# Optimization experiments

Measured on AMD Instinct MI355X. Metric: run time of the kernel, lower is better.

Reference implementation:

```python
import jax, jax.numpy as jnp
import numpy as np

N_QUBITS = 7
N_LAYERS = 2
HILBERT = 2 ** N_QUBITS


def _rx(t):
    c = jnp.cos(t / 2).astype(jnp.complex64)
    s = (-1j * jnp.sin(t / 2)).astype(jnp.complex64)
    return jnp.stack([jnp.stack([c, s]), jnp.stack([s, c])])


def _ry(t):
    c = jnp.cos(t / 2).astype(jnp.complex64)
    s = jnp.sin(t / 2).astype(jnp.complex64)
    return jnp.stack([jnp.stack([c, -s]), jnp.stack([s, c])])


def _rz(t):
    z0 = jnp.exp(-0.5j * t).astype(jnp.complex64)
    z1 = jnp.exp(0.5j * t).astype(jnp.complex64)
    zero = jnp.zeros_like(z0)
    return jnp.stack([jnp.stack([z0, zero]), jnp.stack([zero, z1])])


def _apply_1q(state, U, q):
    # state: [B, 2, 2, ..., 2]; wire q lives on axis q+1 (wire 0 = MSB, PennyLane convention)
    ax = q + 1
    out = jnp.tensordot(U, state, axes=[[1], [ax]])  # new gate axis at 0
    return jnp.moveaxis(out, 0, ax)


def _apply_cnot(state, c, t):
    c_ax, t_ax = c + 1, t + 1
    s0 = jax.lax.index_in_dim(state, 0, c_ax, keepdims=False)
    s1 = jax.lax.index_in_dim(state, 1, c_ax, keepdims=False)
    t2 = t_ax - 1 if t_ax > c_ax else t_ax  # target axis after control axis removed
    s1 = jnp.flip(s1, axis=t2)  # X on target within control=1 block
    return jnp.stack([s0, s1], axis=c_ax)


def setup_inputs() -> dict:
    key = jax.random.key(0)
    k1, k2 = jax.random.split(key)
    x = jax.random.normal(k1, (131072, HILBERT), dtype=jnp.float32)
    weights = jax.random.uniform(k2, (N_LAYERS, N_QUBITS, 3), dtype=jnp.float32) * (2 * np.pi)
    return {"x": x, "weights": weights}


def reference(x, weights):
    B = x.shape[0]
    norms = jnp.maximum(jnp.linalg.norm(x, axis=-1, keepdims=True), 1e-8)
    psi = (x / norms).astype(jnp.complex64)
    state = psi.reshape((B,) + (2,) * N_QUBITS)
    for layer in range(N_LAYERS):
        for q in range(N_QUBITS):
            state = _apply_1q(state, _rx(weights[layer, q, 0]), q)
            state = _apply_1q(state, _ry(weights[layer, q, 1]), q)
            state = _apply_1q(state, _rz(weights[layer, q, 2]), q)
        for q in range(N_QUBITS):
            state = _apply_cnot(state, q, (q + 1) % N_QUBITS)
    probs = jnp.abs(state) ** 2  # real [B, 2,...,2]
    zs = []
    for q in range(N_QUBITS):
        other = tuple(a for a in range(1, N_QUBITS + 1) if a != q + 1)
        p = probs.sum(axis=other)  # [B, 2] marginal of wire q
        zs.append(p[:, 0] - p[:, 1])
    return jnp.stack(zs, axis=-1)  # [B, N_QUBITS]
```

## Files before the change

kernel.cpp:

```cpp
#include <hip/hip_runtime.h>
#include <hip/hip_bf16.h>


typedef __attribute__((ext_vector_type(8)))  short short8;
typedef __attribute__((ext_vector_type(16))) float f32x16;

static __device__ __forceinline__ short f2bf(float f) {
  __bf16 h = (__bf16)f;
  return __builtin_bit_cast(short, h);
}

static __device__ __forceinline__ int widx(int P, int s, int k) {
  return ((((P << 2) + (s >> 5)) * 8 + (k >> 4)) * 64 +
          ((s & 31) + ((k >> 3) & 1) * 32)) * 8 + (k & 7);
}

__global__ void qnn_build_w(const float* __restrict__ wts,
                            short* __restrict__ W) {
  const int k = blockIdx.x;
  const int l = threadIdx.x;

  float c0r = (2 * l     == k) ? 1.f : 0.f, c0i = 0.f;
  float c1r = (2 * l + 1 == k) ? 1.f : 0.f, c1i = 0.f;

  for (int layer = 0; layer < 2; ++layer) {
    for (int q = 0; q < 7; ++q) {
      const float t0 = 0.5f * wts[(layer * 7 + q) * 3 + 0];
      const float t1 = 0.5f * wts[(layer * 7 + q) * 3 + 1];
      const float t2 = 0.5f * wts[(layer * 7 + q) * 3 + 2];
      const float cx = __cosf(t0), sx = __sinf(t0);
      const float cy = __cosf(t1), sy = __sinf(t1);
      const float cz = __cosf(t2), sz = __sinf(t2);
      const float m00r =  cy * cx, m00i =  sy * sx;
      const float m01r = -sy * cx, m01i = -cy * sx;
      const float m10r =  sy * cx, m10i = -cy * sx;
      const float m11r =  cy * cx, m11i = -sy * sx;
      const float g00r = m00r * cz + m00i * sz, g00i = m00i * cz - m00r * sz;
      const float g01r = m01r * cz + m01i * sz, g01i = m01i * cz - m01r * sz;
      const float g10r = m10r * cz - m10i * sz, g10i = m10i * cz + m10r * sz;
      const float g11r = m11r * cz - m11i * sz, g11i = m11i * cz + m11r * sz;

      const int b = 6 - q;
      if (b == 0) {
        const float n0r = g00r*c0r - g00i*c0i + g01r*c1r - g01i*c1i;
        const float n0i = g00r*c0i + g00i*c0r + g01r*c1i + g01i*c1r;
        const float n1r = g10r*c0r - g10i*c0i + g11r*c1r - g11i*c1i;
        const float n1i = g10r*c0i + g10i*c0r + g11r*c1i + g11i*c1r;
        c0r = n0r; c0i = n0i; c1r = n1r; c1i = n1i;
      } else {
        const int xm  = 1 << (b - 1);
        const int myb = (l >> (b - 1)) & 1;
        const float p0r = __shfl_xor(c0r, xm), p0i = __shfl_xor(c0i, xm);
        const float p1r = __shfl_xor(c1r, xm), p1i = __shfl_xor(c1i, xm);
        const float gar = myb ? g11r : g00r, gai = myb ? g11i : g00i;
        const float gbr = myb ? g10r : g01r, gbi = myb ? g10i : g01i;
        const float n0r = gar*c0r - gai*c0i + gbr*p0r - gbi*p0i;
        const float n0i = gar*c0i + gai*c0r + gbr*p0i + gbi*p0r;
        const float n1r = gar*c1r - gai*c1i + gbr*p1r - gbi*p1i;
        const float n1i = gar*c1i + gai*c1r + gbr*p1i + gbi*p1r;
        c0r = n0r; c0i = n0i; c1r = n1r; c1i = n1i;
      }
    }
    #pragma unroll
    for (int q = 0; q < 7; ++q) {
      const int bc = 6 - q;
      const int bt = 6 - ((q + 1) % 7);
      if (bt == 0) {
        if (l & 1) { float tr=c0r, ti=c0i; c0r=c1r; c0i=c1i; c1r=tr; c1i=ti; }
      } else if (bc == 0) {
        c1r = __shfl_xor(c1r, 32);
        c1i = __shfl_xor(c1i, 32);
      } else {
        const int xm = 1 << (bt - 1);
        const float p0r = __shfl_xor(c0r, xm), p0i = __shfl_xor(c0i, xm);
        const float p1r = __shfl_xor(c1r, xm), p1i = __shfl_xor(c1i, xm);
        if ((l >> (bc - 1)) & 1) { c0r=p0r; c0i=p0i; c1r=p1r; c1i=p1i; }
      }
    }
  }

  W[widx(0, 2 * l,     k)] = f2bf(c0r);
  W[widx(0, 2 * l + 1, k)] = f2bf(c1r);
  W[widx(1, 2 * l,     k)] = f2bf(c0i);
  W[widx(1, 2 * l + 1, k)] = f2bf(c1i);
}

__global__ __launch_bounds__(256, 4) void qnn_main(
    const float* __restrict__ x, const short* __restrict__ W,
    float* __restrict__ out) {
  const int tid = threadIdx.x;
  const int l   = tid & 63;
  const int wv  = tid >> 6;
  const int col = l & 31;
  const int h   = l >> 5;

  __shared__ short8 xb[1024];
  __shared__ float  red[4][64][7];

  const int t0 = blockIdx.x;

  float4 fa[4], fb[4];
  #pragma unroll
  for (int i = 0; i < 4; ++i) {
    const int p = i * 256 + tid;
    const int r = p >> 4, q = p & 15;
    const float* gp = x + (size_t)(t0 * 64 + r) * 128 + q * 8;
    fa[i] = *reinterpret_cast<const float4*>(gp);
    fb[i] = *reinterpret_cast<const float4*>(gp + 4);
  }

  short8 A0[8], A1[8];
  #pragma unroll
  for (int j = 0; j < 8; ++j) {
    const int off = ((wv * 8 + j) * 64 + l) * 8;
    A0[j] = *reinterpret_cast<const short8*>(W + off);
    A1[j] = *reinterpret_cast<const short8*>(W + 16384 + off);
  }

  #pragma unroll
  for (int i = 0; i < 4; ++i) {
    const int p = i * 256 + tid;
    const int r = p >> 4, q = p & 15;
    short8 c;
    c[0]=f2bf(fa[i].x); c[1]=f2bf(fa[i].y); c[2]=f2bf(fa[i].z); c[3]=f2bf(fa[i].w);
    c[4]=f2bf(fb[i].x); c[5]=f2bf(fb[i].y); c[6]=f2bf(fb[i].z); c[7]=f2bf(fb[i].w);
    xb[r * 16 + (q ^ (r & 7))] = c;
  }
  asm volatile("s_waitcnt lgkmcnt(0)" ::: "memory");
  __builtin_amdgcn_s_barrier();
  asm volatile("" ::: "memory");

  #pragma unroll
  for (int g = 0; g < 2; ++g) {
    f32x16 acc0 = {0.f,0.f,0.f,0.f,0.f,0.f,0.f,0.f,
                   0.f,0.f,0.f,0.f,0.f,0.f,0.f,0.f};
    f32x16 acc1 = {0.f,0.f,0.f,0.f,0.f,0.f,0.f,0.f,
                   0.f,0.f,0.f,0.f,0.f,0.f,0.f,0.f};
    const int r = g * 32 + col;
    #pragma unroll
    for (int j = 0; j < 8; ++j) {
      const int q = j * 2 + h;
      const short8 bfr = xb[r * 16 + (q ^ (r & 7))];
      acc0 = __builtin_amdgcn_mfma_f32_32x32x16_bf16(A0[j], bfr, acc0, 0, 0, 0);
      acc1 = __builtin_amdgcn_mfma_f32_32x32x16_bf16(A1[j], bfr, acc1, 0, 0, 0);
    }
    float aS[8], aD[8];
    #pragma unroll
    for (int i = 0; i < 8; ++i) {
      const float pe = acc0[2*i]   * acc0[2*i]   + acc1[2*i]   * acc1[2*i];
      const float po = acc0[2*i+1] * acc0[2*i+1] + acc1[2*i+1] * acc1[2*i+1];
      aS[i] = pe + po;
      aD[i] = pe - po;
    }
    float bS[4], bD[4];
    #pragma unroll
    for (int i = 0; i < 4; ++i) {
      bS[i] = aS[2*i] + aS[2*i+1];
      bD[i] = aS[2*i] - aS[2*i+1];
    }
    float u0 = ((aD[0]+aD[1]) + (aD[2]+aD[3])) + ((aD[4]+aD[5]) + (aD[6]+aD[7]));
    float u1 = (bD[0] + bD[1]) + (bD[2] + bD[3]);
    const float cS0 = bS[0] + bS[1], cD0 = bS[0] - bS[1];
    const float cS1 = bS[2] + bS[3], cD1 = bS[2] - bS[3];
    float u3 = cD0 + cD1;
    float u4 = cS0 - cS1;
    float T  = cS0 + cS1;

    const float Tp = __shfl_xor(T, 32);
    const float u2 = h ? (Tp - T) : (T - Tp);
    T += Tp;
    u0 += __shfl_xor(u0, 32);
    u1 += __shfl_xor(u1, 32);
    u3 += __shfl_xor(u3, 32);
    u4 += __shfl_xor(u4, 32);

    if (h == 0) {
      red[wv][r][0] = T;
      red[wv][r][1] = u0;
      red[wv][r][2] = u1;
      red[wv][r][3] = u2;
      red[wv][r][4] = u3;
      red[wv][r][5] = u4;
    }
  }

  asm volatile("s_waitcnt lgkmcnt(0)" ::: "memory");
  __builtin_amdgcn_s_barrier();
  asm volatile("" ::: "memory");

  if (tid < 64) {
    const int c = tid;
    const float T0 = red[0][c][0], T1 = red[1][c][0];
    const float T2 = red[2][c][0], T3 = red[3][c][0];
    const float sT  = (T0 + T1) + (T2 + T3);
    const float inv = 1.0f / sT;
    const float z0 = (T0 + T1) - (T2 + T3);
    const float z1 = (T0 - T1) + (T2 - T3);
    float zr[5];
    #pragma unroll
    for (int i = 0; i < 5; ++i)
      zr[i] = (red[0][c][5-i] + red[1][c][5-i]) +
              (red[2][c][5-i] + red[3][c][5-i]);
    float* o = out + (size_t)(t0 * 64 + c) * 7;
    o[0] = z0 * inv; o[1] = z1 * inv; o[2] = zr[0] * inv; o[3] = zr[1] * inv;
    o[4] = zr[2] * inv; o[5] = zr[3] * inv; o[6] = zr[4] * inv;
  }
}

extern "C" void kernel_launch(void* const* d_in, const int* in_sizes, int n_in,
                              void* d_out, int out_size, void* d_ws, size_t ws_size,
                              hipStream_t stream) {
  const float* x   = (const float*)d_in[0];
  const float* wts = (const float*)d_in[1];
  float* out = (float*)d_out;
  short* W   = (short*)d_ws;

  const int B     = in_sizes[0] / 128;
  const int grid  = B / 64;

  qnn_build_w<<<128, 64, 0, stream>>>(wts, W);
  qnn_main<<<grid, 256, 0, stream>>>(x, W, out);
}
```

Baseline: 24.05 us.

## Double-buffer x tiles in LDS via async global_load_lds across a persistent loop

```diff
diff --git a/kernel.cpp b/kernel.cpp
--- a/kernel.cpp
+++ b/kernel.cpp
@@ -8,6 +8,12 @@
 static __device__ __forceinline__ short f2bf(float f) {
   __bf16 h = (__bf16)f;
   return __builtin_bit_cast(short, h);
+}
+
+static __device__ __forceinline__ void gl16(const void* g, void* l) {
+  __builtin_amdgcn_global_load_lds(
+      (const __attribute__((address_space(1))) void*)g,
+      (__attribute__((address_space(3))) void*)l, 16, 0, 0);
 }
 
 static __device__ __forceinline__ int widx(int P, int s, int k) {
@@ -87,27 +93,18 @@
 
 __global__ __launch_bounds__(256, 4) void qnn_main(
     const float* __restrict__ x, const short* __restrict__ W,
-    float* __restrict__ out) {
+    float* __restrict__ out, int ntiles) {
   const int tid = threadIdx.x;
   const int l   = tid & 63;
   const int wv  = tid >> 6;
   const int col = l & 31;
   const int h   = l >> 5;
 
-  __shared__ short8 xb[1024];
-  __shared__ float  red[4][64][7];
-
-  const int t0 = blockIdx.x;
-
-  float4 fa[4], fb[4];
-  #pragma unroll
-  for (int i = 0; i < 4; ++i) {
-    const int p = i * 256 + tid;
-    const int r = p >> 4, q = p & 15;
-    const float* gp = x + (size_t)(t0 * 64 + r) * 128 + q * 8;
-    fa[i] = *reinterpret_cast<const float4*>(gp);
-    fb[i] = *reinterpret_cast<const float4*>(gp + 4);
-  }
+  __shared__ float xb[2][4096];
+  __shared__ float red[4][32][7];
+
+  const int T0 = blockIdx.x * 4;
+  const int NT = min(4, ntiles - T0);
 
   short8 A0[8], A1[8];
   #pragma unroll
@@ -117,93 +114,119 @@
     A1[j] = *reinterpret_cast<const short8*>(W + 16384 + off);
   }
 
-  #pragma unroll
-  for (int i = 0; i < 4; ++i) {
-    const int p = i * 256 + tid;
-    const int r = p >> 4, q = p & 15;
-    short8 c;
-    c[0]=f2bf(fa[i].x); c[1]=f2bf(fa[i].y); c[2]=f2bf(fa[i].z); c[3]=f2bf(fa[i].w);
-    c[4]=f2bf(fb[i].x); c[5]=f2bf(fb[i].y); c[6]=f2bf(fb[i].z); c[7]=f2bf(fb[i].w);
-    xb[r * 16 + (q ^ (r & 7))] = c;
-  }
-  asm volatile("s_waitcnt lgkmcnt(0)" ::: "memory");
-  __builtin_amdgcn_s_barrier();
-  asm volatile("" ::: "memory");
-
-  #pragma unroll
-  for (int g = 0; g < 2; ++g) {
+  auto ISSUE = [&](int T, int b) {
+    const char* gbase = (const char*)(x + (size_t)T * 32 * 128);
+    char* lbase = (char*)&xb[b][0];
+    #pragma unroll
+    for (int i = 0; i < 4; ++i) {
+      const int d   = i * 4096 + tid * 16;
+      const int r   = d >> 9;
+      const int c16 = (d >> 4) & 31;
+      const int q32 = c16 >> 1, hf = c16 & 1;
+      const int qg  = q32 ^ (r & 7);
+      const int hg  = hf  ^ ((r >> 3) & 1);
+      gl16(gbase + r * 512 + qg * 32 + hg * 16, lbase + d);
+    }
+  };
+
+  if (NT > 0) ISSUE(T0, 0);
+  if (NT > 1) ISSUE(T0 + 1, 1);
+
+  for (int i = 0; i < NT; ++i) {
+    const int p = i & 1;
+
+    if (i + 1 < NT) { asm volatile("s_waitcnt vmcnt(4)" ::: "memory"); }
+    else            { asm volatile("s_waitcnt vmcnt(0)" ::: "memory"); }
+    __builtin_amdgcn_s_barrier();
+    asm volatile("" ::: "memory");
+
     f32x16 acc0 = {0.f,0.f,0.f,0.f,0.f,0.f,0.f,0.f,
                    0.f,0.f,0.f,0.f,0.f,0.f,0.f,0.f};
     f32x16 acc1 = {0.f,0.f,0.f,0.f,0.f,0.f,0.f,0.f,
                    0.f,0.f,0.f,0.f,0.f,0.f,0.f,0.f};
-    const int r = g * 32 + col;
-    #pragma unroll
-    for (int j = 0; j < 8; ++j) {
-      const int q = j * 2 + h;
-      const short8 bfr = xb[r * 16 + (q ^ (r & 7))];
-      acc0 = __builtin_amdgcn_mfma_f32_32x32x16_bf16(A0[j], bfr, acc0, 0, 0, 0);
-      acc1 = __builtin_amdgcn_mfma_f32_32x32x16_bf16(A1[j], bfr, acc1, 0, 0, 0);
-    }
-    float aS[8], aD[8];
-    #pragma unroll
-    for (int i = 0; i < 8; ++i) {
-      const float pe = acc0[2*i]   * acc0[2*i]   + acc1[2*i]   * acc1[2*i];
-      const float po = acc0[2*i+1] * acc0[2*i+1] + acc1[2*i+1] * acc1[2*i+1];
-      aS[i] = pe + po;
-      aD[i] = pe - po;
-    }
-    float bS[4], bD[4];
-    #pragma unroll
-    for (int i = 0; i < 4; ++i) {
-      bS[i] = aS[2*i] + aS[2*i+1];
-      bD[i] = aS[2*i] - aS[2*i+1];
-    }
-    float u0 = ((aD[0]+aD[1]) + (aD[2]+aD[3])) + ((aD[4]+aD[5]) + (aD[6]+aD[7]));
-    float u1 = (bD[0] + bD[1]) + (bD[2] + bD[3]);
-    const float cS0 = bS[0] + bS[1], cD0 = bS[0] - bS[1];
-    const float cS1 = bS[2] + bS[3], cD1 = bS[2] - bS[3];
-    float u3 = cD0 + cD1;
-    float u4 = cS0 - cS1;
-    float T  = cS0 + cS1;
-
-    const float Tp = __shfl_xor(T, 32);
-    const float u2 = h ? (Tp - T) : (T - Tp);
-    T += Tp;
-    u0 += __shfl_xor(u0, 32);
-    u1 += __shfl_xor(u1, 32);
-    u3 += __shfl_xor(u3, 32);
-    u4 += __shfl_xor(u4, 32);
-
-    if (h == 0) {
-      red[wv][r][0] = T;
-      red[wv][r][1] = u0;
-      red[wv][r][2] = u1;
-      red[wv][r][3] = u2;
-      red[wv][r][4] = u3;
-      red[wv][r][5] = u4;
-    }
-  }
-
-  asm volatile("s_waitcnt lgkmcnt(0)" ::: "memory");
-  __builtin_amdgcn_s_barrier();
-  asm volatile("" ::: "memory");
-
-  if (tid < 64) {
-    const int c = tid;
-    const float T0 = red[0][c][0], T1 = red[1][c][0];
-    const float T2 = red[2][c][0], T3 = red[3][c][0];
-    const float sT  = (T0 + T1) + (T2 + T3);
-    const float inv = 1.0f / sT;
-    const float z0 = (T0 + T1) - (T2 + T3);
-    const float z1 = (T0 - T1) + (T2 - T3);
-    float zr[5];
-    #pragma unroll
-    for (int i = 0; i < 5; ++i)
-      zr[i] = (red[0][c][5-i] + red[1][c][5-i]) +
-              (red[2][c][5-i] + red[3][c][5-i]);
-    float* o = out + (size_t)(t0 * 64 + c) * 7;
-    o[0] = z0 * inv; o[1] = z1 * inv; o[2] = zr[0] * inv; o[3] = zr[1] * inv;
-    o[4] = zr[2] * inv; o[5] = zr[3] * inv; o[6] = zr[4] * inv;
+    {
+      const int hb = (col >> 3) & 1;
+      const char* xrow = (const char*)&xb[p][0] + col * 512;
+      #pragma unroll
+      for (int j = 0; j < 8; ++j) {
+        const int qg  = j * 2 + h;
+        const int q32 = qg ^ (col & 7);
+        const float4 f0 = *reinterpret_cast<const float4*>(
+            xrow + q32 * 32 + hb * 16);
+        const float4 f1 = *reinterpret_cast<const float4*>(
+            xrow + q32 * 32 + (hb ^ 1) * 16);
+        short8 bfr;
+        bfr[0]=f2bf(f0.x); bfr[1]=f2bf(f0.y); bfr[2]=f2bf(f0.z); bfr[3]=f2bf(f0.w);
+        bfr[4]=f2bf(f1.x); bfr[5]=f2bf(f1.y); bfr[6]=f2bf(f1.z); bfr[7]=f2bf(f1.w);
+        acc0 = __builtin_amdgcn_mfma_f32_32x32x16_bf16(A0[j], bfr, acc0, 0, 0, 0);
+        acc1 = __builtin_amdgcn_mfma_f32_32x32x16_bf16(A1[j], bfr, acc1, 0, 0, 0);
+      }
+    }
+
+    {
+      float aS[8], aD[8];
+      #pragma unroll
+      for (int i2 = 0; i2 < 8; ++i2) {
+        const float pe = acc0[2*i2]   * acc0[2*i2]   + acc1[2*i2]   * acc1[2*i2];
+        const float po = acc0[2*i2+1] * acc0[2*i2+1] + acc1[2*i2+1] * acc1[2*i2+1];
+        aS[i2] = pe + po;
+        aD[i2] = pe - po;
+      }
+      float bS[4], bD[4];
+      #pragma unroll
+      for (int i2 = 0; i2 < 4; ++i2) {
+        bS[i2] = aS[2*i2] + aS[2*i2+1];
+        bD[i2] = aS[2*i2] - aS[2*i2+1];
+      }
+      float u0 = ((aD[0]+aD[1]) + (aD[2]+aD[3])) + ((aD[4]+aD[5]) + (aD[6]+aD[7]));
+      float u1 = (bD[0] + bD[1]) + (bD[2] + bD[3]);
+      const float cS0 = bS[0] + bS[1], cD0 = bS[0] - bS[1];
+      const float cS1 = bS[2] + bS[3], cD1 = bS[2] - bS[3];
+      float u3 = cD0 + cD1;
+      float u4 = cS0 - cS1;
+      float T  = cS0 + cS1;
+
+      const float Tp = __shfl_xor(T, 32);
+      const float u2 = h ? (Tp - T) : (T - Tp);
+      T += Tp;
+      u0 += __shfl_xor(u0, 32);
+      u1 += __shfl_xor(u1, 32);
+      u3 += __shfl_xor(u3, 32);
+      u4 += __shfl_xor(u4, 32);
+
+      if (h == 0) {
+        red[wv][col][0] = T;
+        red[wv][col][1] = u0;
+        red[wv][col][2] = u1;
+        red[wv][col][3] = u2;
+        red[wv][col][4] = u3;
+        red[wv][col][5] = u4;
+      }
+    }
+
+    asm volatile("s_waitcnt lgkmcnt(0)" ::: "memory");
+    __builtin_amdgcn_s_barrier();
+    asm volatile("" ::: "memory");
+
+    if (tid < 32) {
+      const int c = tid;
+      const float T0v = red[0][c][0], T1v = red[1][c][0];
+      const float T2v = red[2][c][0], T3v = red[3][c][0];
+      const float sT  = (T0v + T1v) + (T2v + T3v);
+      const float inv = 1.0f / sT;
+      const float z0 = (T0v + T1v) - (T2v + T3v);
+      const float z1 = (T0v - T1v) + (T2v - T3v);
+      float zr[5];
+      #pragma unroll
+      for (int i2 = 0; i2 < 5; ++i2)
+        zr[i2] = (red[0][c][5-i2] + red[1][c][5-i2]) +
+                 (red[2][c][5-i2] + red[3][c][5-i2]);
+      float* o = out + (size_t)((T0 + i) * 32 + c) * 7;
+      o[0] = z0 * inv; o[1] = z1 * inv; o[2] = zr[0] * inv; o[3] = zr[1] * inv;
+      o[4] = zr[2] * inv; o[5] = zr[3] * inv; o[6] = zr[4] * inv;
+    }
+
+    if (i + 2 < NT) ISSUE(T0 + i + 2, p);
   }
 }
 
@@ -215,9 +238,10 @@
   float* out = (float*)d_out;
   short* W   = (short*)d_ws;
 
-  const int B     = in_sizes[0] / 128;
-  const int grid  = B / 64;
+  const int B      = in_sizes[0] / 128;
+  const int ntiles = B / 32;
+  const int grid   = (ntiles + 3) / 4;
 
   qnn_build_w<<<128, 64, 0, stream>>>(wts, W);
-  qnn_main<<<grid, 256, 0, stream>>>(x, W, out);
-}
+  qnn_main<<<grid, 256, 0, stream>>>(x, W, out, ntiles);
+}
```

New measurement: 31.37 us. 1.3x slower.

## Stage fp32 input tile into LDS via direct global-to-LDS loads

Applied to the files above, without the earlier changes.

```diff
diff --git a/kernel.cpp b/kernel.cpp
--- a/kernel.cpp
+++ b/kernel.cpp
@@ -8,6 +8,12 @@
 static __device__ __forceinline__ short f2bf(float f) {
   __bf16 h = (__bf16)f;
   return __builtin_bit_cast(short, h);
+}
+
+static __device__ __forceinline__ void gl16(const void* g, void* l) {
+  __builtin_amdgcn_global_load_lds(
+      (const __attribute__((address_space(1))) void*)g,
+      (__attribute__((address_space(3))) void*)l, 16, 0, 0);
 }
 
 static __device__ __forceinline__ int widx(int P, int s, int k) {
@@ -94,20 +100,26 @@
   const int col = l & 31;
   const int h   = l >> 5;
 
-  __shared__ short8 xb[1024];
-  __shared__ float  red[4][64][7];
+  __shared__ float xb[8192];
+  __shared__ float red[4][64][6];
 
   const int t0 = blockIdx.x;
 
-  float4 fa[4], fb[4];
-  #pragma unroll
-  for (int i = 0; i < 4; ++i) {
-    const int p = i * 256 + tid;
-    const int r = p >> 4, q = p & 15;
-    const float* gp = x + (size_t)(t0 * 64 + r) * 128 + q * 8;
-    fa[i] = *reinterpret_cast<const float4*>(gp);
-    fb[i] = *reinterpret_cast<const float4*>(gp + 4);
-  }
+  {
+    const char* gbase = (const char*)(x + (size_t)t0 * 64 * 128);
+    char* lbase = (char*)&xb[0];
+    #pragma unroll
+    for (int i = 0; i < 8; ++i) {
+      const int d   = i * 4096 + tid * 16;
+      const int r   = d >> 9;
+      const int c16 = (d >> 4) & 31;
+      const int q32 = c16 >> 1, hf = c16 & 1;
+      const int qg  = q32 ^ (r & 7);
+      const int hg  = hf  ^ ((r >> 3) & 1);
+      gl16(gbase + r * 512 + qg * 32 + hg * 16, lbase + d);
+    }
+  }
+  asm volatile("" ::: "memory");
 
   short8 A0[8], A1[8];
   #pragma unroll
@@ -117,16 +129,7 @@
     A1[j] = *reinterpret_cast<const short8*>(W + 16384 + off);
   }
 
-  #pragma unroll
-  for (int i = 0; i < 4; ++i) {
-    const int p = i * 256 + tid;
-    const int r = p >> 4, q = p & 15;
-    short8 c;
-    c[0]=f2bf(fa[i].x); c[1]=f2bf(fa[i].y); c[2]=f2bf(fa[i].z); c[3]=f2bf(fa[i].w);
-    c[4]=f2bf(fb[i].x); c[5]=f2bf(fb[i].y); c[6]=f2bf(fb[i].z); c[7]=f2bf(fb[i].w);
-    xb[r * 16 + (q ^ (r & 7))] = c;
-  }
-  asm volatile("s_waitcnt lgkmcnt(0)" ::: "memory");
+  asm volatile("s_waitcnt vmcnt(16)" ::: "memory");
   __builtin_amdgcn_s_barrier();
   asm volatile("" ::: "memory");
 
@@ -136,14 +139,24 @@
                    0.f,0.f,0.f,0.f,0.f,0.f,0.f,0.f};
     f32x16 acc1 = {0.f,0.f,0.f,0.f,0.f,0.f,0.f,0.f,
                    0.f,0.f,0.f,0.f,0.f,0.f,0.f,0.f};
-    const int r = g * 32 + col;
+    const int row = g * 32 + col;
+    const int hb  = (row >> 3) & 1;
+    const char* xrow = (const char*)&xb[0] + row * 512;
     #pragma unroll
     for (int j = 0; j < 8; ++j) {
-      const int q = j * 2 + h;
-      const short8 bfr = xb[r * 16 + (q ^ (r & 7))];
+      const int qg  = j * 2 + h;
+      const int q32 = qg ^ (row & 7);
+      const float4 f0 = *reinterpret_cast<const float4*>(
+          xrow + q32 * 32 + hb * 16);
+      const float4 f1 = *reinterpret_cast<const float4*>(
+          xrow + q32 * 32 + (hb ^ 1) * 16);
+      short8 bfr;
+      bfr[0]=f2bf(f0.x); bfr[1]=f2bf(f0.y); bfr[2]=f2bf(f0.z); bfr[3]=f2bf(f0.w);
+      bfr[4]=f2bf(f1.x); bfr[5]=f2bf(f1.y); bfr[6]=f2bf(f1.z); bfr[7]=f2bf(f1.w);
       acc0 = __builtin_amdgcn_mfma_f32_32x32x16_bf16(A0[j], bfr, acc0, 0, 0, 0);
       acc1 = __builtin_amdgcn_mfma_f32_32x32x16_bf16(A1[j], bfr, acc1, 0, 0, 0);
     }
+
     float aS[8], aD[8];
     #pragma unroll
     for (int i = 0; i < 8; ++i) {
@@ -175,12 +188,12 @@
     u4 += __shfl_xor(u4, 32);
 
     if (h == 0) {
-      red[wv][r][0] = T;
-      red[wv][r][1] = u0;
-      red[wv][r][2] = u1;
-      red[wv][r][3] = u2;
-      red[wv][r][4] = u3;
-      red[wv][r][5] = u4;
+      red[wv][row][0] = T;
+      red[wv][row][1] = u0;
+      red[wv][row][2] = u1;
+      red[wv][row][3] = u2;
+      red[wv][row][4] = u3;
+      red[wv][row][5] = u4;
     }
   }
 
```

New measurement: 26.05 us. 8.3% more time.
